# Kernel optimization log

Hardware: AMD Instinct MI355X
Metric: run time of the kernel (lower is better)

The kernel has to match this reference:

```python
import jax, jax.numpy as jnp
import numpy as np

B, T, LA, L = 4, 32, 32, 512
D, H, C = 2048, 16, 128
KV_DIM = 2048
K = T * LA  # total kv tokens per batch element
EPS = 1e-5


def _ln(x):
    m = jnp.mean(x, axis=-1, keepdims=True)
    v = jnp.var(x, axis=-1, keepdims=True)
    return (x - m) * jax.lax.rsqrt(v + EPS)


def setup_inputs() -> dict:
    key = jax.random.key(0)
    ks = jax.random.split(key, 10)
    s = 1.0 / np.sqrt(D)
    sk = 1.0 / np.sqrt(KV_DIM)
    return {
        "x": jax.random.normal(ks[0], (B, T, LA, KV_DIM), jnp.float32),
        "latents": jax.random.normal(ks[1], (B, L, D), jnp.float32),
        "t_emb": jax.random.normal(ks[2], (B, 3, D), jnp.float32) * 0.02,
        "q_lens": jnp.full((B,), L, dtype=jnp.int32),
        "k_lens": jax.random.randint(ks[3], (B,), K // 2, K + 1).astype(jnp.int32),
        "ln_kv_w": jnp.ones((KV_DIM,), jnp.float32),
        "ln_kv_b": jnp.zeros((KV_DIM,), jnp.float32),
        "ssg": jax.random.normal(ks[4], (1, 3, D), jnp.float32) * s,  # shift_scale_gate param (adaLN=True)
        "Wq": jax.random.normal(ks[5], (D, D), jnp.float32) * s,
        "bq": jnp.zeros((D,), jnp.float32),
        "Wkv": jax.random.normal(ks[6], (KV_DIM, 2 * D), jnp.float32) * sk,
        "bkv": jnp.zeros((2 * D,), jnp.float32),
        "Wo": jax.random.normal(ks[7], (D, D), jnp.float32) * s,
        "bo": jnp.zeros((D,), jnp.float32),
    }


def reference(x, latents, t_emb, q_lens, k_lens, ln_kv_w, ln_kv_b, ssg,
              Wq, bq, Wkv, bkv, Wo, bo):
    # norm_kv (affine LayerNorm over kv_dim)
    xk = _ln(x) * ln_kv_w + ln_kv_b  # (B,T,LA,KV_DIM)
    # AdaLN modulate: shift/scale/gate from t_emb + learned shift_scale_gate
    mod = t_emb + ssg  # (B,3,D)
    shift, scale, gate = mod[:, 0:1], mod[:, 1:2], mod[:, 2:3]  # (B,1,D)
    norm_q = _ln(latents)  # norm_q has no affine when adaLN=True
    lat = norm_q * (1.0 + scale) + shift
    # projections
    q = (lat @ Wq + bq).reshape(B, L, H, C)
    kv = (xk.reshape(B, K, KV_DIM) @ Wkv + bkv)  # (B,K,2D)
    k, v = kv[..., :D], kv[..., D:]
    k = k.reshape(B, K, H, C)
    v = v.reshape(B, K, H, C)
    # varlen attention == per-batch masked attention (keys beyond k_lens masked)
    scores = jnp.einsum("blhc,bkhc->bhlk", q, k) / np.sqrt(C)
    kmask = jnp.arange(K)[None, :] < k_lens[:, None]  # (B,K)
    scores = jnp.where(kmask[:, None, None, :], scores, jnp.finfo(scores.dtype).min)
    attn = jax.nn.softmax(scores, axis=-1)
    out = jnp.einsum("bhlk,bkhc->blhc", attn, v).reshape(B, L, D)
    # queries beyond q_lens are invalid -> zero them (varlen packing semantics)
    qmask = (jnp.arange(L)[None, :] < q_lens[:, None])[..., None]  # (B,L,1)
    out = out * qmask
    return (out @ Wo + bo) * gate
```

## Files before the change

kernel.cpp:

```cpp
#include <hip/hip_runtime.h>

typedef unsigned short u16;
typedef short bf16x8 __attribute__((ext_vector_type(8)));
typedef float f32x4 __attribute__((ext_vector_type(4)));

#define MFMA_BF16(a, b, c) __builtin_amdgcn_mfma_f32_16x16x32_bf16((a), (b), (c), 0, 0, 0)
#define ATT_SCALE 0.08838834764831845f

__device__ __forceinline__ u16 f2bf(float f) {
  union { float f; unsigned int u; } cv;
  cv.f = f;
  unsigned int u = cv.u + 0x7fffu + ((cv.u >> 16) & 1u);
  return (u16)(u >> 16);
}

__device__ __forceinline__ void gload_lds16(const u16* g, u16* l) {
  __builtin_amdgcn_global_load_lds(
      (const __attribute__((address_space(1))) unsigned int*)g,
      (__attribute__((address_space(3))) unsigned int*)l, 16, 0, 0);
}

__global__ __launch_bounds__(256) void prep_kernel(
    const float* __restrict__ x, const float* __restrict__ ln_w,
    const float* __restrict__ ln_b, const float* __restrict__ latents,
    const float* __restrict__ t_emb, const float* __restrict__ ssg,
    const float* __restrict__ Wq, const float* __restrict__ Wo,
    const float* __restrict__ Wkv,
    u16* __restrict__ xk_out, u16* __restrict__ lat_out,
    u16* __restrict__ WqT, u16* __restrict__ WoT, u16* __restrict__ WkvT)
{
  __shared__ float shmem[32 * 33];
  const int blk = blockIdx.x;
  const int tid = threadIdx.x;
  if (blk < 6144) {
    const bool is_x = blk < 4096;
    const int row = is_x ? blk : blk - 4096;
    const float* src = is_x ? (x + (size_t)row * 2048) : (latents + (size_t)row * 2048);
    const float4* xr = (const float4*)src;
    float4 v0 = xr[tid];
    float4 v1 = xr[tid + 256];
    float sum = v0.x + v0.y + v0.z + v0.w + v1.x + v1.y + v1.z + v1.w;
    float sq  = v0.x*v0.x + v0.y*v0.y + v0.z*v0.z + v0.w*v0.w
              + v1.x*v1.x + v1.y*v1.y + v1.z*v1.z + v1.w*v1.w;
    #pragma unroll
    for (int off = 32; off > 0; off >>= 1) {
      sum += __shfl_xor(sum, off);
      sq  += __shfl_xor(sq, off);
    }
    if ((tid & 63) == 0) { shmem[tid >> 6] = sum; shmem[(tid >> 6) + 4] = sq; }
    __syncthreads();
    sum = shmem[0] + shmem[1] + shmem[2] + shmem[3];
    sq  = shmem[4] + shmem[5] + shmem[6] + shmem[7];
    const float mean = sum * (1.0f / 2048.0f);
    const float var  = sq * (1.0f / 2048.0f) - mean * mean;
    const float rstd = rsqrtf(var + 1e-5f);
    if (is_x) {
      const float4* w4 = (const float4*)ln_w;
      const float4* b4 = (const float4*)ln_b;
      ushort4* orow = (ushort4*)(xk_out + (size_t)row * 2048);
      #pragma unroll
      for (int j = 0; j < 2; ++j) {
        const int idx = tid + j * 256;
        const float4 v = j ? v1 : v0;
        const float4 ww = w4[idx];
        const float4 bb = b4[idx];
        ushort4 o;
        o.x = f2bf((v.x - mean) * rstd * ww.x + bb.x);
        o.y = f2bf((v.y - mean) * rstd * ww.y + bb.y);
        o.z = f2bf((v.z - mean) * rstd * ww.z + bb.z);
        o.w = f2bf((v.w - mean) * rstd * ww.w + bb.w);
        orow[idx] = o;
      }
    } else {
      const int bidx = row >> 9;
      const float4* te = (const float4*)(t_emb + (size_t)bidx * 3 * 2048);
      const float4* sg = (const float4*)ssg;
      ushort4* orow = (ushort4*)(lat_out + (size_t)row * 2048);
      #pragma unroll
      for (int j = 0; j < 2; ++j) {
        const int idx = tid + j * 256;
        const float4 v = j ? v1 : v0;
        const float4 t0 = te[idx];
        const float4 t1 = te[512 + idx];
        const float4 s0 = sg[idx];
        const float4 s1 = sg[512 + idx];
        ushort4 o;
        o.x = f2bf(((v.x - mean) * rstd) * (1.0f + t1.x + s1.x) + (t0.x + s0.x));
        o.y = f2bf(((v.y - mean) * rstd) * (1.0f + t1.y + s1.y) + (t0.y + s0.y));
        o.z = f2bf(((v.z - mean) * rstd) * (1.0f + t1.z + s1.z) + (t0.z + s0.z));
        o.w = f2bf(((v.w - mean) * rstd) * (1.0f + t1.w + s1.w) + (t0.w + s0.w));
        orow[idx] = o;
      }
    }
  } else {
    int t = blk - 6144;
    const float* in;
    u16* outp;
    int C, cx, ry;
    if (t < 4096)      { in = Wq;  outp = WqT;  C = 2048; cx = t & 63;  ry = t >> 6; }
    else if (t < 8192) { t -= 4096; in = Wo;  outp = WoT;  C = 2048; cx = t & 63;  ry = t >> 6; }
    else               { t -= 8192; in = Wkv; outp = WkvT; C = 4096; cx = t & 127; ry = t >> 7; }
    float (*tile)[33] = (float(*)[33])shmem;
    const int R = 2048;
    const int c0 = cx * 32;
    const int r0 = ry * 32;
    const int tx = tid & 31;
    const int ty = tid >> 5;
    #pragma unroll
    for (int i = 0; i < 4; ++i)
      tile[ty + i * 8][tx] = in[(size_t)(r0 + ty + i * 8) * C + c0 + tx];
    __syncthreads();
    #pragma unroll
    for (int i = 0; i < 4; ++i)
      outp[(size_t)(c0 + ty + i * 8) * R + r0 + tx] = f2bf(tile[tx][ty + i * 8]);
  }
}

template<int BM, int BN>
__global__ __launch_bounds__(256) void gemm_bf16_kernel(
    const u16* __restrict__ A, const u16* __restrict__ BT,
    int Kd, int mode,
    const float* __restrict__ bias,
    u16* __restrict__ out_q, u16* __restrict__ out_k, u16* __restrict__ out_vT,
    float* __restrict__ out_f,
    const float* __restrict__ t_emb, const float* __restrict__ ssg,
    const int* __restrict__ k_lens)
{
  constexpr int TI = BM / 32;
  constexpr int TJ = BN / 32;
  __shared__ u16 As[BM][32];
  __shared__ u16 Bs[BN][32];
  const int tid  = threadIdx.x;
  const int lane = tid & 63;
  const int wv   = tid >> 6;
  const int wm   = wv & 1, wn = wv >> 1;
  const int quad = lane >> 4, lq = lane & 15;
  const int m0 = blockIdx.y * BM, n0 = blockIdx.x * BN;

  f32x4 acc[TI][TJ];
  #pragma unroll
  for (int i = 0; i < TI; ++i)
    #pragma unroll
    for (int j = 0; j < TJ; ++j)
      acc[i][j] = (f32x4){0.f, 0.f, 0.f, 0.f};

  int kiters = Kd;
  if (mode == 1 && (m0 & 1023) >= k_lens[m0 >> 10]) kiters = 0;

  const int lr = lane >> 2;
  const int lc = (lane & 3) << 3;
  const u16* gA = A  + (size_t)(m0 + lr) * Kd + lc;
  const u16* gB = BT + (size_t)(n0 + lr) * Kd + lc;

  for (int k0 = 0; k0 < kiters; k0 += 32) {
    __syncthreads();
    #pragma unroll
    for (int p = 0; p < BM / 64; ++p) {
      const int ch = wv + (p << 2);
      gload_lds16(gA + (size_t)(ch * 16) * Kd + k0, &As[ch * 16][0]);
    }
    #pragma unroll
    for (int p = 0; p < BN / 64; ++p) {
      const int ch = wv + (p << 2);
      gload_lds16(gB + (size_t)(ch * 16) * Kd + k0, &Bs[ch * 16][0]);
    }
    __syncthreads();
    bf16x8 av[TI], bv[TJ];
    #pragma unroll
    for (int i = 0; i < TI; ++i)
      av[i] = *(const bf16x8*)&As[wm * (BM / 2) + i * 16 + lq][quad * 8];
    #pragma unroll
    for (int j = 0; j < TJ; ++j)
      bv[j] = *(const bf16x8*)&Bs[wn * (BN / 2) + j * 16 + lq][quad * 8];
    #pragma unroll
    for (int i = 0; i < TI; ++i)
      #pragma unroll
      for (int j = 0; j < TJ; ++j)
        acc[i][j] = MFMA_BF16(av[i], bv[j], acc[i][j]);
  }

  #pragma unroll
  for (int i = 0; i < TI; ++i) {
    const int mlb = m0 + wm * (BM / 2) + i * 16 + quad * 4;
    #pragma unroll
    for (int j = 0; j < TJ; ++j) {
      const int n = n0 + wn * (BN / 2) + j * 16 + lq;
      const float bs = bias[n];
      if (mode == 0) {
        const int h = n >> 7, c = n & 127;
        #pragma unroll
        for (int rr = 0; rr < 4; ++rr) {
          const int m = mlb + rr;
          const int bb = m >> 9, l = m & 511;
          out_q[((size_t)(bb * 16 + h) * 512 + l) * 128 + c] =
              f2bf((acc[i][j][rr] + bs) * ATT_SCALE);
        }
      } else if (mode == 1) {
        if (n < 2048) {
          const int h = n >> 7, c = n & 127;
          #pragma unroll
          for (int rr = 0; rr < 4; ++rr) {
            const int m = mlb + rr;
            const int bb = m >> 10, kk = m & 1023;
            out_k[((size_t)(bb * 16 + h) * 1024 + kk) * 128 + c] = f2bf(acc[i][j][rr] + bs);
          }
        } else {
          const int n2 = n - 2048;
          const int h = n2 >> 7, c = n2 & 127;
          #pragma unroll
          for (int rr = 0; rr < 4; ++rr) {
            const int m = mlb + rr;
            const int bb = m >> 10, kk = m & 1023;
            out_vT[((size_t)(bb * 16 + h) * 128 + c) * 1024 + kk] = f2bf(acc[i][j][rr] + bs);
          }
        }
      } else {
        #pragma unroll
        for (int rr = 0; rr < 4; ++rr) {
          const int m = mlb + rr;
          const int bb = m >> 9;
          const float g = t_emb[((size_t)bb * 3 + 2) * 2048 + n] + ssg[2 * 2048 + n];
          out_f[(size_t)m * 2048 + n] = (acc[i][j][rr] + bs) * g;
        }
      }
    }
  }
}

__global__ __launch_bounds__(256) void attn_kernel(
    const u16* __restrict__ qb, const u16* __restrict__ kb,
    const u16* __restrict__ vT, const int* __restrict__ k_lens,
    const int* __restrict__ q_lens, u16* __restrict__ ao)
{
  __shared__ u16 Ks[64][132];
  __shared__ u16 Vs[128][68];
  __shared__ u16 Ps[64][68];
  const int tid  = threadIdx.x;
  const int w    = tid >> 6;
  const int lane = tid & 63;
  const int quad = lane >> 4, lq = lane & 15;
  const int bh = blockIdx.y;
  const int b  = bh >> 4;
  const int l0 = blockIdx.x * 64;
  const int kl = k_lens[b];
  const int ql = q_lens[b];

  bf16x8 qf[4];
  {
    const u16* qp = qb + ((size_t)bh * 512 + l0 + w * 16 + lq) * 128 + quad * 8;
    #pragma unroll
    for (int ks = 0; ks < 4; ++ks)
      qf[ks] = *(const bf16x8*)(qp + ks * 32);
  }

  const int krow = tid >> 4;
  const int kcol = tid & 15;
  const u16* kg = kb + ((size_t)bh * 1024 + krow) * 128 + kcol * 8;
  const int vrow = tid >> 3;
  const int vcol = tid & 7;
  const u16* vg = vT + (size_t)bh * 128 * 1024 + (size_t)vrow * 1024 + vcol * 8;

  f32x4 o[8];
  #pragma unroll
  for (int j = 0; j < 8; ++j) o[j] = (f32x4){0.f, 0.f, 0.f, 0.f};
  float mrun[4], lrun[4];
  #pragma unroll
  for (int rr = 0; rr < 4; ++rr) { mrun[rr] = -__builtin_inff(); lrun[rr] = 0.f; }

  const int nkt = (kl + 63) >> 6;
  for (int kt = 0; kt < nkt; ++kt) {
    const int k0 = kt * 64;
    uint4 kd[4], vd[4];
    #pragma unroll
    for (int p = 0; p < 4; ++p)
      kd[p] = *(const uint4*)(kg + (size_t)(k0 + p * 16) * 128);
    #pragma unroll
    for (int p = 0; p < 4; ++p)
      vd[p] = *(const uint4*)(vg + (size_t)p * 32 * 1024 + k0);
    __syncthreads();
    #pragma unroll
    for (int p = 0; p < 4; ++p)
      *(uint4*)&Ks[krow + p * 16][kcol * 8] = kd[p];
    #pragma unroll
    for (int p = 0; p < 4; ++p)
      *(uint4*)&Vs[vrow + p * 32][vcol * 8] = vd[p];
    __syncthreads();

    f32x4 s[4];
    #pragma unroll
    for (int ct = 0; ct < 4; ++ct) {
      s[ct] = (f32x4){0.f, 0.f, 0.f, 0.f};
      #pragma unroll
      for (int ks = 0; ks < 4; ++ks) {
        const bf16x8 kf = *(const bf16x8*)&Ks[ct * 16 + lq][ks * 32 + quad * 8];
        s[ct] = MFMA_BF16(qf[ks], kf, s[ct]);
      }
    }
    #pragma unroll
    for (int ct = 0; ct < 4; ++ct) {
      const bool valid = (k0 + ct * 16 + lq) < kl;
      #pragma unroll
      for (int rr = 0; rr < 4; ++rr)
        s[ct][rr] = valid ? s[ct][rr] : -__builtin_inff();
    }
    float mnew[4], alpha[4], rs[4];
    #pragma unroll
    for (int rr = 0; rr < 4; ++rr) {
      float tm = fmaxf(fmaxf(s[0][rr], s[1][rr]), fmaxf(s[2][rr], s[3][rr]));
      tm = fmaxf(tm, __shfl_xor(tm, 1));
      tm = fmaxf(tm, __shfl_xor(tm, 2));
      tm = fmaxf(tm, __shfl_xor(tm, 4));
      tm = fmaxf(tm, __shfl_xor(tm, 8));
      const float mn = fmaxf(mrun[rr], tm);
      alpha[rr] = __expf(mrun[rr] - mn);
      mrun[rr] = mn;
      mnew[rr] = mn;
      rs[rr] = 0.f;
    }
    #pragma unroll
    for (int ct = 0; ct < 4; ++ct)
      #pragma unroll
      for (int rr = 0; rr < 4; ++rr) {
        const float p = __expf(s[ct][rr] - mnew[rr]);
        s[ct][rr] = p;
        rs[rr] += p;
      }
    #pragma unroll
    for (int rr = 0; rr < 4; ++rr) {
      float t = rs[rr];
      t += __shfl_xor(t, 1);
      t += __shfl_xor(t, 2);
      t += __shfl_xor(t, 4);
      t += __shfl_xor(t, 8);
      lrun[rr] = lrun[rr] * alpha[rr] + t;
    }
    #pragma unroll
    for (int j = 0; j < 8; ++j)
      #pragma unroll
      for (int rr = 0; rr < 4; ++rr)
        o[j][rr] *= alpha[rr];

    #pragma unroll
    for (int ct = 0; ct < 4; ++ct)
      #pragma unroll
      for (int rr = 0; rr < 4; ++rr)
        Ps[w * 16 + quad * 4 + rr][ct * 16 + lq] = f2bf(s[ct][rr]);

    bf16x8 pf[2];
    pf[0] = *(const bf16x8*)&Ps[w * 16 + lq][quad * 8];
    pf[1] = *(const bf16x8*)&Ps[w * 16 + lq][32 + quad * 8];

    #pragma unroll
    for (int j = 0; j < 8; ++j) {
      #pragma unroll
      for (int kk = 0; kk < 2; ++kk) {
        const bf16x8 vf = *(const bf16x8*)&Vs[j * 16 + lq][kk * 32 + quad * 8];
        o[j] = MFMA_BF16(pf[kk], vf, o[j]);
      }
    }
  }

  const int h = bh & 15;
  #pragma unroll
  for (int rr = 0; rr < 4; ++rr) {
    const int row = l0 + w * 16 + quad * 4 + rr;
    const float inv = (row < ql) ? (1.0f / lrun[rr]) : 0.0f;
    u16* op = ao + ((size_t)b * 512 + row) * 2048 + h * 128 + lq;
    #pragma unroll
    for (int j = 0; j < 8; ++j)
      op[j * 16] = f2bf(o[j][rr] * inv);
  }
}

extern "C" void kernel_launch(void* const* d_in, const int* in_sizes, int n_in,
                              void* d_out, int out_size, void* d_ws, size_t ws_size,
                              hipStream_t stream) {
  (void)in_sizes; (void)n_in; (void)out_size; (void)ws_size;
  const float* x       = (const float*)d_in[0];
  const float* latents = (const float*)d_in[1];
  const float* t_emb   = (const float*)d_in[2];
  const int*   q_lens  = (const int*)d_in[3];
  const int*   k_lens  = (const int*)d_in[4];
  const float* ln_w    = (const float*)d_in[5];
  const float* ln_b    = (const float*)d_in[6];
  const float* ssg     = (const float*)d_in[7];
  const float* Wq      = (const float*)d_in[8];
  const float* bq      = (const float*)d_in[9];
  const float* Wkv     = (const float*)d_in[10];
  const float* bkv     = (const float*)d_in[11];
  const float* Wo      = (const float*)d_in[12];
  const float* bo      = (const float*)d_in[13];
  float* out = (float*)d_out;

  u16* ws = (u16*)d_ws;
  const size_t MEG = (size_t)1 << 20;
  u16* WqT  = ws;
  u16* WoT  = ws + 4  * MEG;
  u16* WkvT = ws + 8  * MEG;
  u16* xk   = ws + 16 * MEG;
  u16* lat  = ws + 24 * MEG;
  u16* qb   = ws + 28 * MEG;
  u16* kbuf = ws + 32 * MEG;
  u16* vTb  = ws + 40 * MEG;
  u16* aob  = ws + 48 * MEG;

  prep_kernel<<<dim3(22528), dim3(256), 0, stream>>>(
      x, ln_w, ln_b, latents, t_emb, ssg, Wq, Wo, Wkv,
      xk, lat, WqT, WoT, WkvT);

  gemm_bf16_kernel<64, 128><<<dim3(16, 32), dim3(256), 0, stream>>>(
      lat, WqT, 2048, 0, bq, qb, nullptr, nullptr, nullptr, nullptr, nullptr, k_lens);
  gemm_bf16_kernel<128, 128><<<dim3(32, 32), dim3(256), 0, stream>>>(
      xk, WkvT, 2048, 1, bkv, nullptr, kbuf, vTb, nullptr, nullptr, nullptr, k_lens);

  attn_kernel<<<dim3(8, 64), dim3(256), 0, stream>>>(qb, kbuf, vTb, k_lens, q_lens, aob);

  gemm_bf16_kernel<64, 128><<<dim3(16, 32), dim3(256), 0, stream>>>(
      aob, WoT, 2048, 2, bo, nullptr, nullptr, nullptr, out, t_emb, ssg, k_lens);
}
```

Measured before the change: 434.9 us.

## Double-buffer GEMM LDS tiles, prefetch attention K/V, swizzle workgroup order

The GEMM kernel now double-buffers its A/B LDS tiles, issuing the next k-slice's global-to-LDS loads before computing on the current one, with a single barrier per iteration. Workgroup IDs are remapped with an XCD-style swizzle to change which blocks run together and share cache. The V-transpose epilogue now writes four consecutive bf16 values as one vector store. The attention kernel loads the next K/V tile into registers while computing on the current tile, hiding global latency at the cost of extra registers and LDS.

```diff
diff --git a/kernel.cpp b/kernel.cpp
--- a/kernel.cpp
+++ b/kernel.cpp
@@ -128,14 +128,21 @@
 {
   constexpr int TI = BM / 32;
   constexpr int TJ = BN / 32;
-  __shared__ u16 As[BM][32];
-  __shared__ u16 Bs[BN][32];
+  __shared__ u16 As[2][BM][32];
+  __shared__ u16 Bs[2][BN][32];
   const int tid  = threadIdx.x;
   const int lane = tid & 63;
   const int wv   = tid >> 6;
   const int wm   = wv & 1, wn = wv >> 1;
   const int quad = lane >> 4, lq = lane & 15;
-  const int m0 = blockIdx.y * BM, n0 = blockIdx.x * BN;
+
+  const int nbx = gridDim.x, nby = gridDim.y;
+  const int nwg = nbx * nby;
+  const int hw  = blockIdx.y * nbx + blockIdx.x;
+  const int logical = (hw & 7) * (nwg >> 3) + (hw >> 3);
+  const int bx = logical / nby;
+  const int by = logical - bx * nby;
+  const int m0 = by * BM, n0 = bx * BN;
 
   f32x4 acc[TI][TJ];
   #pragma unroll
@@ -152,31 +159,40 @@
   const u16* gA = A  + (size_t)(m0 + lr) * Kd + lc;
   const u16* gB = BT + (size_t)(n0 + lr) * Kd + lc;
 
-  for (int k0 = 0; k0 < kiters; k0 += 32) {
-    __syncthreads();
+  auto stage = [&](int buf, int k0) {
     #pragma unroll
     for (int p = 0; p < BM / 64; ++p) {
       const int ch = wv + (p << 2);
-      gload_lds16(gA + (size_t)(ch * 16) * Kd + k0, &As[ch * 16][0]);
+      gload_lds16(gA + (size_t)(ch * 16) * Kd + k0, &As[buf][ch * 16][0]);
     }
     #pragma unroll
     for (int p = 0; p < BN / 64; ++p) {
       const int ch = wv + (p << 2);
-      gload_lds16(gB + (size_t)(ch * 16) * Kd + k0, &Bs[ch * 16][0]);
-    }
+      gload_lds16(gB + (size_t)(ch * 16) * Kd + k0, &Bs[buf][ch * 16][0]);
+    }
+  };
+
+  if (kiters > 0) {
+    int cur = 0;
+    stage(0, 0);
     __syncthreads();
-    bf16x8 av[TI], bv[TJ];
-    #pragma unroll
-    for (int i = 0; i < TI; ++i)
-      av[i] = *(const bf16x8*)&As[wm * (BM / 2) + i * 16 + lq][quad * 8];
-    #pragma unroll
-    for (int j = 0; j < TJ; ++j)
-      bv[j] = *(const bf16x8*)&Bs[wn * (BN / 2) + j * 16 + lq][quad * 8];
-    #pragma unroll
-    for (int i = 0; i < TI; ++i)
+    for (int k0 = 0; k0 < kiters; k0 += 32) {
+      if (k0 + 32 < kiters) stage(cur ^ 1, k0 + 32);
+      bf16x8 av[TI], bv[TJ];
+      #pragma unroll
+      for (int i = 0; i < TI; ++i)
+        av[i] = *(const bf16x8*)&As[cur][wm * (BM / 2) + i * 16 + lq][quad * 8];
       #pragma unroll
       for (int j = 0; j < TJ; ++j)
-        acc[i][j] = MFMA_BF16(av[i], bv[j], acc[i][j]);
+        bv[j] = *(const bf16x8*)&Bs[cur][wn * (BN / 2) + j * 16 + lq][quad * 8];
+      #pragma unroll
+      for (int i = 0; i < TI; ++i)
+        #pragma unroll
+        for (int j = 0; j < TJ; ++j)
+          acc[i][j] = MFMA_BF16(av[i], bv[j], acc[i][j]);
+      __syncthreads();
+      cur ^= 1;
+    }
   }
 
   #pragma unroll
@@ -207,12 +223,13 @@
         } else {
           const int n2 = n - 2048;
           const int h = n2 >> 7, c = n2 & 127;
-          #pragma unroll
-          for (int rr = 0; rr < 4; ++rr) {
-            const int m = mlb + rr;
-            const int bb = m >> 10, kk = m & 1023;
-            out_vT[((size_t)(bb * 16 + h) * 128 + c) * 1024 + kk] = f2bf(acc[i][j][rr] + bs);
-          }
+          const int bb = mlb >> 10, kk = mlb & 1023;
+          ushort4 o4;
+          o4.x = f2bf(acc[i][j][0] + bs);
+          o4.y = f2bf(acc[i][j][1] + bs);
+          o4.z = f2bf(acc[i][j][2] + bs);
+          o4.w = f2bf(acc[i][j][3] + bs);
+          *(ushort4*)&out_vT[((size_t)(bb * 16 + h) * 128 + c) * 1024 + kk] = o4;
         }
       } else {
         #pragma unroll
@@ -268,15 +285,15 @@
   for (int rr = 0; rr < 4; ++rr) { mrun[rr] = -__builtin_inff(); lrun[rr] = 0.f; }
 
   const int nkt = (kl + 63) >> 6;
+  uint4 kd[4], vd[4];
+  #pragma unroll
+  for (int p = 0; p < 4; ++p)
+    kd[p] = *(const uint4*)(kg + (size_t)(p * 16) * 128);
+  #pragma unroll
+  for (int p = 0; p < 4; ++p)
+    vd[p] = *(const uint4*)(vg + (size_t)p * 32 * 1024);
+
   for (int kt = 0; kt < nkt; ++kt) {
-    const int k0 = kt * 64;
-    uint4 kd[4], vd[4];
-    #pragma unroll
-    for (int p = 0; p < 4; ++p)
-      kd[p] = *(const uint4*)(kg + (size_t)(k0 + p * 16) * 128);
-    #pragma unroll
-    for (int p = 0; p < 4; ++p)
-      vd[p] = *(const uint4*)(vg + (size_t)p * 32 * 1024 + k0);
     __syncthreads();
     #pragma unroll
     for (int p = 0; p < 4; ++p)
@@ -286,6 +303,17 @@
       *(uint4*)&Vs[vrow + p * 32][vcol * 8] = vd[p];
     __syncthreads();
 
+    if (kt + 1 < nkt) {
+      const int kn = (kt + 1) * 64;
+      #pragma unroll
+      for (int p = 0; p < 4; ++p)
+        kd[p] = *(const uint4*)(kg + (size_t)(kn + p * 16) * 128);
+      #pragma unroll
+      for (int p = 0; p < 4; ++p)
+        vd[p] = *(const uint4*)(vg + (size_t)p * 32 * 1024 + kn);
+    }
+
+    const int k0 = kt * 64;
     f32x4 s[4];
     #pragma unroll
     for (int ct = 0; ct < 4; ++ct) {
```

Result: slower. 444.4 us (+2.2%).
